# Kernel optimization log

Measured on AMD Instinct MI355X. Metric: run time of the kernel, lower is better.

Reference implementation:

```python
import jax, jax.numpy as jnp
import numpy as np

K = 7        # kernel_size
DIL = 2      # dilation (hardcoded in module)
PAD = 6      # padding, keeps spatial dims with stride=1
G = 8        # groups (group_channels = 16)


def setup_inputs() -> dict:
    key = jax.random.key(0)
    ks = jax.random.split(key, 5)
    B, C, H, W = 4, 128, 64, 64
    Cr = C // 4                      # red_ratio = 4
    KKG = K * K * G                  # 392
    return {
        "x": jax.random.normal(ks[0], (B, C, H, W), jnp.float32),
        "w_reduce": jax.random.normal(ks[1], (Cr, C), jnp.float32) * 0.05,
        "b_reduce": jax.random.normal(ks[2], (Cr,), jnp.float32) * 0.05,
        "w_span": jax.random.normal(ks[3], (KKG, Cr), jnp.float32) * 0.05,
        "b_span": jax.random.normal(ks[4], (KKG,), jnp.float32) * 0.05,
    }


def reference(x, w_reduce, b_reduce, w_span, b_span):
    B, C, H, W = x.shape
    Cg = C // G
    # kernel generation: two 1x1 convs (pointwise matmuls over channel dim)
    red = jnp.einsum('bchw,oc->bohw', x, w_reduce) + b_reduce[None, :, None, None]
    ker = jnp.einsum('bohw,ko->bkhw', red, w_span) + b_span[None, :, None, None]
    ker = ker.reshape(B, G, K * K, H, W)          # [B, G, KK, H, W]
    # unfold: dilated KxK patches, stride 1, 'same' output size
    xp = jnp.pad(x, ((0, 0), (0, 0), (PAD, PAD), (PAD, PAD)))
    patches = jnp.stack(
        [xp[:, :, i * DIL:i * DIL + H, j * DIL:j * DIL + W]
         for i in range(K) for j in range(K)], axis=2)  # [B, C, KK, H, W]
    patches = patches.reshape(B, G, Cg, K * K, H, W)
    # per-pixel dynamic kernel multiply + sum over window
    out = jnp.einsum('bgckhw,bgkhw->bgchw', patches, ker)
    return out.reshape(B, C, H, W)
```

## Files before the change

kernel.cpp:

```cpp
#include <hip/hip_runtime.h>


#define HW 4096
#define NC 128
#define NR 32
#define KK 49
#define KSB 144

typedef __attribute__((ext_vector_type(8))) short short8;
typedef __attribute__((ext_vector_type(4))) float f32x4;

__device__ __forceinline__ unsigned short f2bf(float f) {
  unsigned int u = __float_as_uint(f);
  u = (u + 0x7fffu + ((u >> 16) & 1u)) >> 16;
  return (unsigned short)u;
}
__device__ __forceinline__ float bf2f(unsigned short u) {
  return __uint_as_float(((unsigned int)u) << 16);
}

__global__ __launch_bounds__(256) void red_gen(
    const float* __restrict__ x, const float* __restrict__ w_reduce,
    const float* __restrict__ b_reduce, unsigned short* __restrict__ red_bf) {
  __shared__ float xs[NC][64];
  int t = threadIdx.x;
  int blk = blockIdx.x;
  int b = blk >> 7;
  int sub = blk & 127;
  int row = sub >> 1;
  int oh = sub & 1;
  int p0 = row * 64;

  const float* xb = x + b * NC * HW + p0;
  int fx = t & 15;
  int c0 = t >> 4;
#pragma unroll
  for (int r = 0; r < 8; ++r) {
    int c = c0 + 16 * r;
    *(float4*)(&xs[c][fx * 4]) = *(const float4*)(xb + c * HW + fx * 4);
  }
  __syncthreads();

  int px = t & 63;
  int wv = __builtin_amdgcn_readfirstlane(t >> 6);
  int ob = oh * 16 + wv * 4;
  const float* wq = w_reduce + ob * NC;

  float acc[4];
#pragma unroll
  for (int j = 0; j < 4; ++j) acc[j] = b_reduce[ob + j];

#pragma unroll 8
  for (int k = 0; k < NC; ++k) {
    float xk = xs[k][px];
#pragma unroll
    for (int j = 0; j < 4; ++j) acc[j] += xk * wq[j * NC + k];
  }

  union { unsigned long long v; unsigned short u[4]; } pk;
#pragma unroll
  for (int j = 0; j < 4; ++j) pk.u[j] = f2bf(acc[j]);
  *(unsigned long long*)(red_bf + ((size_t)(b * HW) + p0 + px) * NR + ob) = pk.v;
}

__global__ __launch_bounds__(256) void inv_fused(
    const float* __restrict__ x, const unsigned short* __restrict__ red_bf,
    const float* __restrict__ w_span, const float* __restrict__ b_span,
    float* __restrict__ out) {
  __shared__ unsigned short kvs_bf[KK * KSB];
  __shared__ short wlds[64 * NR];
  __shared__ float bsl[64];

  int orig = blockIdx.x;
  int blk = (orig & 7) * 128 + (orig >> 3);
  int hp = blk & 31;
  int g = (blk >> 5) & 7;
  int b = blk >> 8;
  int tid = threadIdx.x;
  int h0 = hp * 2;
  int p0 = h0 * 64;

  const float* wg = w_span + g * KK * NR;
#pragma unroll
  for (int it = 0; it < 8; ++it) {
    int idx = it * 256 + tid;
    wlds[idx] = (idx < KK * NR) ? (short)f2bf(wg[idx]) : (short)0;
  }
  if (tid < 64) bsl[tid] = (tid < KK) ? b_span[g * KK + tid] : 0.f;
  __syncthreads();

  int l = tid & 63;
  int wv = __builtin_amdgcn_readfirstlane(tid >> 6);
  int quad = l >> 4;
  int mn = l & 15;

  short8 af[4];
#pragma unroll
  for (int tt = 0; tt < 4; ++tt)
    af[tt] = *(const short8*)(&wlds[(tt * 16 + mn) * NR + quad * 8]);

  f32x4 ci[4];
#pragma unroll
  for (int tt = 0; tt < 4; ++tt) {
#pragma unroll
    for (int r = 0; r < 4; ++r) ci[tt][r] = bsl[tt * 16 + quad * 4 + r];
  }

  const unsigned short* rb =
      red_bf + ((size_t)b * HW + p0 + wv * 32 + mn) * NR + quad * 8;
#pragma unroll
  for (int nt = 0; nt < 2; ++nt) {
    short8 bf = *(const short8*)(rb + (size_t)nt * 16 * NR);
    f32x4 d0 = __builtin_amdgcn_mfma_f32_16x16x32_bf16(af[0], bf, ci[0], 0, 0, 0);
    f32x4 d1 = __builtin_amdgcn_mfma_f32_16x16x32_bf16(af[1], bf, ci[1], 0, 0, 0);
    f32x4 d2 = __builtin_amdgcn_mfma_f32_16x16x32_bf16(af[2], bf, ci[2], 0, 0, 0);
    f32x4 d3 = __builtin_amdgcn_mfma_f32_16x16x32_bf16(af[3], bf, ci[3], 0, 0, 0);
    int pxl = wv * 32 + nt * 16 + mn;
    int r = pxl >> 6, col = pxl & 63;
    int base = r * 72 + col;
#pragma unroll
    for (int rg = 0; rg < 4; ++rg) {
      kvs_bf[(0 * 16 + quad * 4 + rg) * KSB + base] = f2bf(d0[rg]);
      kvs_bf[(1 * 16 + quad * 4 + rg) * KSB + base] = f2bf(d1[rg]);
      kvs_bf[(2 * 16 + quad * 4 + rg) * KSB + base] = f2bf(d2[rg]);
    }
    if (quad == 0) kvs_bf[48 * KSB + base] = f2bf(d3[0]);
  }
  __syncthreads();

  int c = tid >> 4;
  int sub = tid & 15;
  int r = sub >> 3;
  int oct = sub & 7;

  const float* xc = x + ((size_t)(b * NC + g * 16 + c)) * HW + 8 * oct - 8;
  int mo0 = 0, mo1 = 4, mo4 = 16, mo5 = 20;
  if (oct == 0) { mo0 = 8; mo1 = 12; }
  if (oct == 7) { mo4 = 8; mo5 = 12; }

  float2 a0 = {0.f, 0.f}, a1 = {0.f, 0.f}, a2 = {0.f, 0.f}, a3 = {0.f, 0.f};

#pragma unroll
  for (int i = 0; i < 7; ++i) {
    int rbase = h0 + 2 * i - 6;
    if (rbase < 0 || rbase > 62) continue;
    const float* pr = xc + (size_t)(rbase + r) * 64;
    float xr[24];
    float4 v;
    v = *(const float4*)(pr + mo0); xr[0]=v.x; xr[1]=v.y; xr[2]=v.z; xr[3]=v.w;
    v = *(const float4*)(pr + mo1); xr[4]=v.x; xr[5]=v.y; xr[6]=v.z; xr[7]=v.w;
    v = *(const float4*)(pr + 8);   xr[8]=v.x; xr[9]=v.y; xr[10]=v.z; xr[11]=v.w;
    v = *(const float4*)(pr + 12);  xr[12]=v.x; xr[13]=v.y; xr[14]=v.z; xr[15]=v.w;
    v = *(const float4*)(pr + mo4); xr[16]=v.x; xr[17]=v.y; xr[18]=v.z; xr[19]=v.w;
    v = *(const float4*)(pr + mo5); xr[20]=v.x; xr[21]=v.y; xr[22]=v.z; xr[23]=v.w;
    if (oct == 0) { xr[2]=0.f; xr[3]=0.f; xr[4]=0.f; xr[5]=0.f; xr[6]=0.f; xr[7]=0.f; }
    if (oct == 7) { xr[16]=0.f; xr[17]=0.f; xr[18]=0.f; xr[19]=0.f; xr[20]=0.f; xr[21]=0.f; }
#pragma unroll
    for (int j = 0; j < 7; ++j) {
      union { short8 v; unsigned short u[8]; } kv;
      kv.v = *(const short8*)(&kvs_bf[(i * 7 + j) * KSB + r * 72 + 8 * oct]);
      a0.x = fmaf(xr[2 + 2 * j], bf2f(kv.u[0]), a0.x);
      a0.y = fmaf(xr[3 + 2 * j], bf2f(kv.u[1]), a0.y);
      a1.x = fmaf(xr[4 + 2 * j], bf2f(kv.u[2]), a1.x);
      a1.y = fmaf(xr[5 + 2 * j], bf2f(kv.u[3]), a1.y);
      a2.x = fmaf(xr[6 + 2 * j], bf2f(kv.u[4]), a2.x);
      a2.y = fmaf(xr[7 + 2 * j], bf2f(kv.u[5]), a2.y);
      a3.x = fmaf(xr[8 + 2 * j], bf2f(kv.u[6]), a3.x);
      a3.y = fmaf(xr[9 + 2 * j], bf2f(kv.u[7]), a3.y);
    }
  }

  int h = h0 + r;
  float* op = out + (size_t)(b * NC + g * 16 + c) * HW + h * 64 + 8 * oct;
  *(float4*)op = make_float4(a0.x, a0.y, a1.x, a1.y);
  *(float4*)(op + 4) = make_float4(a2.x, a2.y, a3.x, a3.y);
}

extern "C" void kernel_launch(void* const* d_in, const int* in_sizes, int n_in,
                              void* d_out, int out_size, void* d_ws, size_t ws_size,
                              hipStream_t stream) {
  const float* x        = (const float*)d_in[0];
  const float* w_reduce = (const float*)d_in[1];
  const float* b_reduce = (const float*)d_in[2];
  const float* w_span   = (const float*)d_in[3];
  const float* b_span   = (const float*)d_in[4];
  float* out = (float*)d_out;

  unsigned short* red_bf = (unsigned short*)d_ws;

  red_gen<<<512, 256, 0, stream>>>(x, w_reduce, b_reduce, red_bf);
  inv_fused<<<1024, 256, 0, stream>>>(x, red_bf, w_span, b_span, out);
}
```

Baseline: 86.02 us.

## Fuse reduction and dynamic-kernel stages into one cooperative launch with grid sync

Merges the two kernels into a single cooperative kernel. The first 512 blocks compute the reduced features, then a grid-wide sync runs, then all 1024 blocks perform the involution, with shared memory overlaid through a union. This is meant to remove the second launch and the gap between kernels. In exchange it adds grid-sync overhead and needs all 1024 blocks co-resident (4 per CU on 256 CUs), falling back to two launches if the cooperative launch fails.

```diff
diff --git a/kernel.cpp b/kernel.cpp
--- a/kernel.cpp
+++ b/kernel.cpp
@@ -1,5 +1,8 @@
 #include <hip/hip_runtime.h>
-
+#include <hip/hip_cooperative_groups.h>
+
+
+namespace cg = cooperative_groups;
 
 #define HW 4096
 #define NC 128
@@ -19,12 +22,20 @@
   return __uint_as_float(((unsigned int)u) << 16);
 }
 
-__global__ __launch_bounds__(256) void red_gen(
-    const float* __restrict__ x, const float* __restrict__ w_reduce,
-    const float* __restrict__ b_reduce, unsigned short* __restrict__ red_bf) {
-  __shared__ float xs[NC][64];
+union SmemU {
+  float xs[NC][64];
+  struct {
+    unsigned short kvs_bf[KK * KSB];
+    short wlds[64 * NR];
+    float bsl[64];
+  } inv;
+};
+
+__device__ __forceinline__ void red_body(
+    SmemU* sm, const float* __restrict__ x,
+    const float* __restrict__ w_reduce, const float* __restrict__ b_reduce,
+    unsigned short* __restrict__ red_bf, int blk) {
   int t = threadIdx.x;
-  int blk = blockIdx.x;
   int b = blk >> 7;
   int sub = blk & 127;
   int row = sub >> 1;
@@ -37,7 +48,7 @@
 #pragma unroll
   for (int r = 0; r < 8; ++r) {
     int c = c0 + 16 * r;
-    *(float4*)(&xs[c][fx * 4]) = *(const float4*)(xb + c * HW + fx * 4);
+    *(float4*)(&sm->xs[c][fx * 4]) = *(const float4*)(xb + c * HW + fx * 4);
   }
   __syncthreads();
 
@@ -52,7 +63,7 @@
 
 #pragma unroll 8
   for (int k = 0; k < NC; ++k) {
-    float xk = xs[k][px];
+    float xk = sm->xs[k][px];
 #pragma unroll
     for (int j = 0; j < 4; ++j) acc[j] += xk * wq[j * NC + k];
   }
@@ -63,15 +74,15 @@
   *(unsigned long long*)(red_bf + ((size_t)(b * HW) + p0 + px) * NR + ob) = pk.v;
 }
 
-__global__ __launch_bounds__(256) void inv_fused(
-    const float* __restrict__ x, const unsigned short* __restrict__ red_bf,
+__device__ __forceinline__ void inv_body(
+    SmemU* sm, const float* __restrict__ x,
+    const unsigned short* __restrict__ red_bf,
     const float* __restrict__ w_span, const float* __restrict__ b_span,
-    float* __restrict__ out) {
-  __shared__ unsigned short kvs_bf[KK * KSB];
-  __shared__ short wlds[64 * NR];
-  __shared__ float bsl[64];
-
-  int orig = blockIdx.x;
+    float* __restrict__ out, int orig) {
+  unsigned short* kvs_bf = sm->inv.kvs_bf;
+  short* wlds = sm->inv.wlds;
+  float* bsl = sm->inv.bsl;
+
   int blk = (orig & 7) * 128 + (orig >> 3);
   int hp = blk & 31;
   int g = (blk >> 5) & 7;
@@ -176,6 +187,33 @@
   *(float4*)(op + 4) = make_float4(a2.x, a2.y, a3.x, a3.y);
 }
 
+__global__ __launch_bounds__(256, 4) void inv_coop(
+    const float* __restrict__ x, const float* __restrict__ w_reduce,
+    const float* __restrict__ b_reduce, const float* __restrict__ w_span,
+    const float* __restrict__ b_span, unsigned short* __restrict__ red_bf,
+    float* __restrict__ out) {
+  __shared__ SmemU sm;
+  int orig = blockIdx.x;
+  if (orig < 512) red_body(&sm, x, w_reduce, b_reduce, red_bf, orig);
+  cg::this_grid().sync();
+  inv_body(&sm, x, red_bf, w_span, b_span, out, orig);
+}
+
+__global__ __launch_bounds__(256) void red_gen(
+    const float* __restrict__ x, const float* __restrict__ w_reduce,
+    const float* __restrict__ b_reduce, unsigned short* __restrict__ red_bf) {
+  __shared__ SmemU sm;
+  red_body(&sm, x, w_reduce, b_reduce, red_bf, blockIdx.x);
+}
+
+__global__ __launch_bounds__(256) void inv_fused(
+    const float* __restrict__ x, const unsigned short* __restrict__ red_bf,
+    const float* __restrict__ w_span, const float* __restrict__ b_span,
+    float* __restrict__ out) {
+  __shared__ SmemU sm;
+  inv_body(&sm, x, red_bf, w_span, b_span, out, blockIdx.x);
+}
+
 extern "C" void kernel_launch(void* const* d_in, const int* in_sizes, int n_in,
                               void* d_out, int out_size, void* d_ws, size_t ws_size,
                               hipStream_t stream) {
@@ -188,6 +226,12 @@
 
   unsigned short* red_bf = (unsigned short*)d_ws;
 
-  red_gen<<<512, 256, 0, stream>>>(x, w_reduce, b_reduce, red_bf);
-  inv_fused<<<1024, 256, 0, stream>>>(x, red_bf, w_span, b_span, out);
-}
+  void* args[] = {(void*)&x, (void*)&w_reduce, (void*)&b_reduce,
+                  (void*)&w_span, (void*)&b_span, (void*)&red_bf, (void*)&out};
+  hipError_t e = hipLaunchCooperativeKernel((void*)inv_coop, dim3(1024),
+                                            dim3(256), args, 0, stream);
+  if (e != hipSuccess) {
+    red_gen<<<512, 256, 0, stream>>>(x, w_reduce, b_reduce, red_bf);
+    inv_fused<<<1024, 256, 0, stream>>>(x, red_bf, w_span, b_span, out);
+  }
+}
```

Measured after the change: 207.8 us. +141.5%, slower.
